# Performance work log

Hardware: AMD Instinct MI355X
Metric: run time of the kernel (lower is better)

The kernel has to match this reference:

```python
import jax, jax.numpy as jnp
import numpy as np

N_NODES = 50000
N_EDGES = 800000
D_IN = 128
D_HID = 128
D_OUT = 64


def sage_conv(x, edge_index, W_l, b_l, W_r):
    # PyG SAGEConv (mean aggr): out = lin_l(mean_{j in N(i)} x_j) + lin_r(x_i)
    src, dst = edge_index[0], edge_index[1]
    msgs = x[src]  # [E, d] gather of source-node features
    summed = jax.ops.segment_sum(msgs, dst, num_segments=x.shape[0])
    deg = jax.ops.segment_sum(jnp.ones((edge_index.shape[1],), x.dtype), dst,
                              num_segments=x.shape[0])
    agg = summed / jnp.maximum(deg, 1.0)[:, None]  # nodes w/o in-edges -> 0
    return agg @ W_l + b_l + x @ W_r


def setup_inputs() -> dict:
    key = jax.random.key(0)
    ks = jax.random.split(key, 12)
    x = jax.random.normal(ks[0], (N_NODES, D_IN), dtype=jnp.float32)
    edge_index = jax.random.randint(ks[1], (2, N_EDGES), 0, N_NODES, dtype=jnp.int32)

    def glorot(k, shape):
        fan_in, fan_out = shape
        lim = (6.0 / (fan_in + fan_out)) ** 0.5
        return jax.random.uniform(k, shape, jnp.float32, -lim, lim)

    dims = [(D_IN, D_HID), (D_HID, D_HID), (D_HID, D_OUT)]
    params = {}
    for i, (din, dout) in enumerate(dims):
        params[f"Wl{i}"] = glorot(ks[2 + 3 * i], (din, dout))
        params[f"bl{i}"] = jnp.zeros((dout,), jnp.float32)
        params[f"Wr{i}"] = glorot(ks[3 + 3 * i], (din, dout))
    return {"x": x, "edge_index": edge_index, **params}


def reference(x, edge_index, Wl0, bl0, Wr0, Wl1, bl1, Wr1, Wl2, bl2, Wr2):
    # eval mode: dropout is identity
    h = jax.nn.relu(sage_conv(x, edge_index, Wl0, bl0, Wr0))
    h = jax.nn.relu(sage_conv(h, edge_index, Wl1, bl1, Wr1))
    out = sage_conv(h, edge_index, Wl2, bl2, Wr2)
    return out
```

## Files before the change

### kernel.cpp

```cpp
#include <hip/hip_runtime.h>

#define NN 50000
#define NE 800000
#define DK 128
#define NN_PAD 50048

#define SW 7
#define SUBCAP 20
#define CAP2 64

#define NPB 128
#define NBKT 391
#define BKTCAP 4096

#define GEMM_GRID 391

typedef __attribute__((ext_vector_type(8))) short bf16x8;
typedef __attribute__((ext_vector_type(4))) float f32x4;
typedef __attribute__((ext_vector_type(2))) int   i32x2;
typedef __attribute__((ext_vector_type(4))) int   i32x4;
typedef __attribute__((ext_vector_type(4))) unsigned u32x4;
typedef __attribute__((ext_vector_type(8))) unsigned short u16x8;

__device__ inline unsigned short f2bf(float f) {
    unsigned u = __builtin_bit_cast(unsigned, f);
    u = (u + 0x7FFFu + ((u >> 16) & 1u)) >> 16;
    return (unsigned short)u;
}
__device__ inline float bfhi2f(unsigned u) {
    return __builtin_bit_cast(float, u & 0xFFFF0000u);
}
__device__ inline float bflo2f(unsigned u) {
    return __builtin_bit_cast(float, u << 16);
}
__device__ inline int clampn(int v) {
    return v >= NN ? NN - 1 : v;
}
__device__ inline void acc16(float* acc, u32x4 v) {
    acc[0] += bflo2f(v.x); acc[1] += bfhi2f(v.x);
    acc[2] += bflo2f(v.y); acc[3] += bfhi2f(v.y);
    acc[4] += bflo2f(v.z); acc[5] += bfhi2f(v.z);
    acc[6] += bflo2f(v.w); acc[7] += bfhi2f(v.w);
}
__device__ inline int xcd_swz(int b, int nwg) {
    int q = nwg >> 3, r = nwg & 7;
    int xc = b & 7, y = b >> 3;
    return (xc < r ? xc * (q + 1) : r * (q + 1) + (xc - r) * q) + y;
}


__global__ __launch_bounds__(256) void partition_edges(const int* __restrict__ src,
                                                       const int* __restrict__ dst,
                                                       int* __restrict__ gcount,
                                                       unsigned* __restrict__ bucketbuf) {
    __shared__ int hist[NBKT];
    __shared__ int cur[NBKT];
    __shared__ int base[NBKT];
    int tid = threadIdx.x;
    for (int i = tid; i < NBKT; i += 256) { hist[i] = 0; cur[i] = 0; }
    __syncthreads();

    unsigned rec[8];
    int bkt[8];
    int e0 = (blockIdx.x * 256 + tid) * 8;
    bool valid = e0 < NE;
    if (valid) {
        i32x4 sa = __builtin_nontemporal_load((const i32x4*)(src + e0));
        i32x4 sb = __builtin_nontemporal_load((const i32x4*)(src + e0 + 4));
        i32x4 da = __builtin_nontemporal_load((const i32x4*)(dst + e0));
        i32x4 db = __builtin_nontemporal_load((const i32x4*)(dst + e0 + 4));
        int ss[8] = {sa.x, sa.y, sa.z, sa.w, sb.x, sb.y, sb.z, sb.w};
        int dd[8] = {da.x, da.y, da.z, da.w, db.x, db.y, db.z, db.w};
        #pragma unroll
        for (int k = 0; k < 8; ++k) {
            bkt[k] = dd[k] >> 7;
            rec[k] = (unsigned)ss[k] | ((unsigned)(dd[k] & 127) << 16);
            atomicAdd(&hist[bkt[k]], 1);
        }
    }
    __syncthreads();
    for (int i = tid; i < NBKT; i += 256)
        base[i] = atomicAdd(&gcount[i], hist[i]);
    __syncthreads();
    if (valid) {
        #pragma unroll
        for (int k = 0; k < 8; ++k) {
            int pos = base[bkt[k]] + atomicAdd(&cur[bkt[k]], 1);
            if (pos < BKTCAP)
                bucketbuf[(size_t)bkt[k] * BKTCAP + pos] = rec[k];
        }
    }
}

__global__ __launch_bounds__(256) void build_lists(const int* __restrict__ gcount,
                                                   const unsigned* __restrict__ bucketbuf,
                                                   unsigned short* __restrict__ eidx2,
                                                   int* __restrict__ deg) {
    __shared__ unsigned short list[NPB * CAP2];
    __shared__ int cnt[NPB * 8];
    __shared__ int cur[NPB * 8];
    __shared__ int off_[NPB * 8];
    int b = blockIdx.x, tid = threadIdx.x;
    int n0 = b << 7;
    int cntE = gcount[b];
    if (cntE > BKTCAP) cntE = BKTCAP;

    for (int i = tid; i < NPB * 8; i += 256) { cnt[i] = 0; cur[i] = 0; }
    u32x4* l4 = (u32x4*)list;
    for (int i = tid; i < NPB * CAP2 / 8; i += 256)
        l4[i] = (u32x4){0u, 0u, 0u, 0u};
    __syncthreads();

    const unsigned* bb = bucketbuf + (size_t)b * BKTCAP;
    for (int i = tid; i < cntE; i += 256) {
        unsigned r = bb[i];
        int nl = r >> 16;
        int w  = (r & 0xFFFFu) >> 13;
        atomicAdd(&cnt[nl * 8 + w], 1);
    }
    __syncthreads();

    if (tid < NPB) {
        int run = 0, dt = 0;
        #pragma unroll
        for (int w = 0; w < SW; ++w) {
            int c = cnt[tid * 8 + w];
            dt += c;
            off_[tid * 8 + w] = run;
            run += (c < SUBCAP) ? c : SUBCAP;
        }
        if (n0 + tid < NN) deg[n0 + tid] = dt;
    }
    __syncthreads();

    for (int i = tid; i < cntE; i += 256) {
        unsigned r = bb[i];
        int s  = (int)(r & 0xFFFFu);
        int nl = r >> 16;
        int w  = s >> 13;
        int slot = atomicAdd(&cur[nl * 8 + w], 1);
        int pos  = off_[nl * 8 + w] + slot;
        if (slot < SUBCAP && pos < CAP2)
            list[nl * CAP2 + pos] = (unsigned short)s;
    }
    __syncthreads();

    int nvalid = NN - n0;
    if (nvalid > NPB) nvalid = NPB;
    u32x4* out4 = (u32x4*)(eidx2 + (size_t)n0 * CAP2);
    for (int i = tid; i < nvalid * (CAP2 / 8); i += 256)
        __builtin_nontemporal_store(l4[i], out4 + i);
}

__global__ __launch_bounds__(256) void prep(const float* __restrict__ x,
                                            unsigned short* __restrict__ xb,
                                            const float* __restrict__ Wl0,
                                            const float* __restrict__ Wr0,
                                            unsigned short* __restrict__ Wp0,
                                            const float* __restrict__ Wl1,
                                            const float* __restrict__ Wr1,
                                            unsigned short* __restrict__ Wp1,
                                            const float* __restrict__ Wl2,
                                            unsigned short* __restrict__ Wp2l,
                                            const float* __restrict__ Wr2,
                                            unsigned short* __restrict__ Wp2r,
                                            int* __restrict__ gcount) {
    int b = blockIdx.x;
    if (b < NN_PAD * DK / 8 / 256) {
        long long i = ((long long)b * 256 + threadIdx.x) * 8;
        if (i < (long long)NN * DK) {
            f32x4 a = __builtin_nontemporal_load((const f32x4*)(x + i));
            f32x4 c = __builtin_nontemporal_load((const f32x4*)(x + i + 4));
            union { unsigned short us[8]; u32x4 u4; } o;
            o.us[0] = f2bf(a.x); o.us[1] = f2bf(a.y); o.us[2] = f2bf(a.z); o.us[3] = f2bf(a.w);
            o.us[4] = f2bf(c.x); o.us[5] = f2bf(c.y); o.us[6] = f2bf(c.z); o.us[7] = f2bf(c.w);
            *(u32x4*)(xb + i) = o.u4;
        } else {
            *(u32x4*)(xb + i) = (u32x4){0u, 0u, 0u, 0u};
        }
        return;
    }
    b -= NN_PAD * DK / 8 / 256;
    if (b < 32) {
        const float* Wl = (b < 16) ? Wl0 : Wl1;
        const float* Wr = (b < 16) ? Wr0 : Wr1;
        unsigned short* Wp = (b < 16) ? Wp0 : Wp1;
        int tid = (b & 15) * 256 + threadIdx.x;
        int l  = tid & 63;
        int ks = (tid >> 6) & 7;
        int nt = tid >> 9;
        int n  = nt * 16 + (l & 15);
        int kb = ks * 32 + (l >> 4) * 8;
        union { unsigned short us[8]; u32x4 u4; } o;
        #pragma unroll
        for (int j = 0; j < 8; ++j) {
            int k = kb + j;
            float w = (k < 128) ? Wl[k * 128 + n] : Wr[(k - 128) * 128 + n];
            o.us[j] = f2bf(w);
        }
        *(u32x4*)(Wp + (size_t)tid * 8) = o.u4;
        return;
    }
    b -= 32;
    if (b < 8) {
        const float* W = (b < 4) ? Wl2 : Wr2;
        unsigned short* Wp = (b < 4) ? Wp2l : Wp2r;
        int tid = (b & 3) * 256 + threadIdx.x;
        int l  = tid & 63;
        int ks = (tid >> 6) & 3;
        int nt = tid >> 8;
        int n  = nt * 16 + (l & 15);
        int kb = ks * 32 + (l >> 4) * 8;
        union { unsigned short us[8]; u32x4 u4; } o;
        #pragma unroll
        for (int j = 0; j < 8; ++j) o.us[j] = f2bf(W[(kb + j) * 64 + n]);
        *(u32x4*)(Wp + (size_t)tid * 8) = o.u4;
        return;
    }
    for (int i = threadIdx.x; i < NBKT; i += 256) gcount[i] = 0;
}

template <bool P2OUT>
__global__ __launch_bounds__(256) void fused_layer(const unsigned short* __restrict__ h,
                                                   const unsigned short* __restrict__ eidx2,
                                                   const int* __restrict__ deg,
                                                   const unsigned short* __restrict__ Wpack,
                                                   const float* __restrict__ bias,
                                                   unsigned short* __restrict__ out,
                                                   const unsigned short* __restrict__ Wp2,
                                                   unsigned short* __restrict__ P2) {
    constexpr int RS = 136;
    __shared__ unsigned short Alds[128 * RS];
    int tid = threadIdx.x;
    int bid = xcd_swz(blockIdx.x, GEMM_GRID);
    int node0 = bid * 128;

    {
        int g = tid >> 4, lane = tid & 15;
        const u32x4* h4 = (const u32x4*)h;
        for (int pass = 0; pass < 8; ++pass) {
            int nl = pass * 16 + g;
            int node = node0 + nl;
            int d = (node < NN) ? deg[node] : 0;
            int cap = (d < CAP2) ? d : CAP2;
            const unsigned short* el = eidx2 + (size_t)node * CAP2;
            float acc[8] = {0.f, 0.f, 0.f, 0.f, 0.f, 0.f, 0.f, 0.f};
            int j = 0;
            for (; j + 7 < cap; j += 8) {
                u16x8 i8 = *(const u16x8*)(el + j);
                u32x4 v[8];
                #pragma unroll
                for (int q = 0; q < 8; ++q)
                    v[q] = h4[(size_t)clampn((int)i8[q]) * 16 + lane];
                #pragma unroll
                for (int q = 0; q < 8; ++q) acc16(acc, v[q]);
            }
            for (; j + 3 < cap; j += 4) {
                u32x4 v[4];
                #pragma unroll
                for (int q = 0; q < 4; ++q)
                    v[q] = h4[(size_t)clampn((int)el[j + q]) * 16 + lane];
                #pragma unroll
                for (int q = 0; q < 4; ++q) acc16(acc, v[q]);
            }
            for (; j < cap; ++j)
                acc16(acc, h4[(size_t)clampn((int)el[j]) * 16 + lane]);
            float rd = 1.0f / (float)(d > 0 ? d : 1);
            union { unsigned short us[8]; u32x4 u4; } o;
            #pragma unroll
            for (int k = 0; k < 8; ++k) o.us[k] = f2bf(acc[k] * rd);
            *(u32x4*)&Alds[nl * RS + lane * 8] = o.u4;
        }
    }
    __syncthreads();

    int wave = tid >> 6, lane = tid & 63;
    int m = lane & 15, quad = lane >> 4;
    int r0 = wave * 16;
    const unsigned short* a0p  = &Alds[(r0 + m) * RS + quad * 8];
    const unsigned short* hrow = h + (size_t)(node0 + r0 + m) * 128 + quad * 8;

    f32x4 acc0[8] = {};
    f32x4 acc1[8] = {};
    #pragma unroll
    for (int ks = 0; ks < 8; ++ks) {
        bf16x8 a0, a1;
        if (ks < 4) {
            a0 = *(const bf16x8*)(a0p + ks * 32);
            a1 = *(const bf16x8*)(a0p + 64 * RS + ks * 32);
        } else {
            a0 = *(const bf16x8*)(hrow + (ks - 4) * 32);
            a1 = *(const bf16x8*)(hrow + 64 * 128 + (ks - 4) * 32);
        }
        #pragma unroll
        for (int nt = 0; nt < 8; ++nt) {
            bf16x8 bfr = *(const bf16x8*)&Wpack[((size_t)(nt * 8 + ks) * 64 + lane) * 8];
            acc0[nt] = __builtin_amdgcn_mfma_f32_16x16x32_bf16(a0, bfr, acc0[nt], 0, 0, 0);
            acc1[nt] = __builtin_amdgcn_mfma_f32_16x16x32_bf16(a1, bfr, acc1[nt], 0, 0, 0);
        }
    }

    #pragma unroll
    for (int t = 0; t < 2; ++t) {
        #pragma unroll
        for (int nt = 0; nt < 8; ++nt) {
            int n = nt * 16 + m;
            float bv = bias[n];
            #pragma unroll
            for (int r = 0; r < 4; ++r) {
                int rl = t * 64 + r0 + quad * 4 + r;
                float v = fmaxf((t == 0 ? acc0[nt][r] : acc1[nt][r]) + bv, 0.f);
                unsigned short us = f2bf(v);
                out[(size_t)(node0 + rl) * 128 + n] = us;
                if constexpr (P2OUT) Alds[rl * RS + n] = us;
            }
        }
    }

    if constexpr (P2OUT) {
        f32x4 p0[4] = {};
        f32x4 p1[4] = {};
        #pragma unroll
        for (int ks = 0; ks < 4; ++ks) {
            bf16x8 a0 = *(const bf16x8*)&Alds[(r0 + m) * RS + ks * 32 + quad * 8];
            bf16x8 a1 = *(const bf16x8*)&Alds[(64 + r0 + m) * RS + ks * 32 + quad * 8];
            #pragma unroll
            for (int nt = 0; nt < 4; ++nt) {
                bf16x8 bfr = *(const bf16x8*)&Wp2[((size_t)(nt * 4 + ks) * 64 + lane) * 8];
                p0[nt] = __builtin_amdgcn_mfma_f32_16x16x32_bf16(a0, bfr, p0[nt], 0, 0, 0);
                p1[nt] = __builtin_amdgcn_mfma_f32_16x16x32_bf16(a1, bfr, p1[nt], 0, 0, 0);
            }
        }
        #pragma unroll
        for (int t = 0; t < 2; ++t) {
            #pragma unroll
            for (int nt = 0; nt < 4; ++nt) {
                int n = nt * 16 + m;
                #pragma unroll
                for (int r = 0; r < 4; ++r) {
                    int rl = t * 64 + r0 + quad * 4 + r;
                    P2[(size_t)(node0 + rl) * 64 + n] =
                        f2bf(t == 0 ? p0[nt][r] : p1[nt][r]);
                }
            }
        }
    }
}

__global__ __launch_bounds__(256) void fused_final(const unsigned short* __restrict__ h,
                                                   const unsigned short* __restrict__ P2,
                                                   const unsigned short* __restrict__ eidx2,
                                                   const int* __restrict__ deg,
                                                   const unsigned short* __restrict__ Wp2r,
                                                   const float* __restrict__ bias,
                                                   float* __restrict__ outp) {
    constexpr int RS2 = 72;
    __shared__ unsigned short Plds[128 * RS2];
    int tid = threadIdx.x;
    int bid = xcd_swz(blockIdx.x, GEMM_GRID);
    int node0 = bid * 128;

    {
        int g = tid >> 3, lane = tid & 7;
        const u32x4* p4 = (const u32x4*)P2;
        for (int pass = 0; pass < 4; ++pass) {
            int nl = pass * 32 + g;
            int node = node0 + nl;
            int d = (node < NN) ? deg[node] : 0;
            int cap = (d < CAP2) ? d : CAP2;
            const unsigned short* el = eidx2 + (size_t)node * CAP2;
            float acc[8] = {0.f, 0.f, 0.f, 0.f, 0.f, 0.f, 0.f, 0.f};
            int j = 0;
            for (; j + 7 < cap; j += 8) {
                u16x8 i8 = *(const u16x8*)(el + j);
                u32x4 v[8];
                #pragma unroll
                for (int q = 0; q < 8; ++q)
                    v[q] = p4[(size_t)clampn((int)i8[q]) * 8 + lane];
                #pragma unroll
                for (int q = 0; q < 8; ++q) acc16(acc, v[q]);
            }
            for (; j + 3 < cap; j += 4) {
                u32x4 v[4];
                #pragma unroll
                for (int q = 0; q < 4; ++q)
                    v[q] = p4[(size_t)clampn((int)el[j + q]) * 8 + lane];
                #pragma unroll
                for (int q = 0; q < 4; ++q) acc16(acc, v[q]);
            }
            for (; j < cap; ++j)
                acc16(acc, p4[(size_t)clampn((int)el[j]) * 8 + lane]);
            float rd = 1.0f / (float)(d > 0 ? d : 1);
            union { unsigned short us[8]; u32x4 u4; } o;
            #pragma unroll
            for (int k = 0; k < 8; ++k) o.us[k] = f2bf(acc[k] * rd);
            *(u32x4*)&Plds[nl * RS2 + lane * 8] = o.u4;
        }
    }
    __syncthreads();

    int wave = tid >> 6, lane = tid & 63;
    int m = lane & 15, quad = lane >> 4;
    int r0 = wave * 16;
    const unsigned short* hrow = h + (size_t)(node0 + r0 + m) * 128 + quad * 8;

    f32x4 acc0[4] = {};
    f32x4 acc1[4] = {};
    #pragma unroll
    for (int ks = 0; ks < 4; ++ks) {
        bf16x8 a0 = *(const bf16x8*)(hrow + ks * 32);
        bf16x8 a1 = *(const bf16x8*)(hrow + ks * 32 + 64 * 128);
        #pragma unroll
        for (int nt = 0; nt < 4; ++nt) {
            bf16x8 bfr = *(const bf16x8*)&Wp2r[((size_t)(nt * 4 + ks) * 64 + lane) * 8];
            acc0[nt] = __builtin_amdgcn_mfma_f32_16x16x32_bf16(a0, bfr, acc0[nt], 0, 0, 0);
            acc1[nt] = __builtin_amdgcn_mfma_f32_16x16x32_bf16(a1, bfr, acc1[nt], 0, 0, 0);
        }
    }

    #pragma unroll
    for (int t = 0; t < 2; ++t) {
        #pragma unroll
        for (int nt = 0; nt < 4; ++nt) {
            int n = nt * 16 + m;
            float bv = bias[n];
            #pragma unroll
            for (int r = 0; r < 4; ++r) {
                int rl = t * 64 + r0 + quad * 4 + r;
                int row = node0 + rl;
                if (row < NN) {
                    float av = bflo2f((unsigned)Plds[rl * RS2 + n]);
                    outp[(size_t)row * 64 + n] =
                        (t == 0 ? acc0[nt][r] : acc1[nt][r]) + bv + av;
                }
            }
        }
    }
}


static inline size_t align256(size_t x) { return (x + 255) & ~(size_t)255; }

extern "C" void kernel_launch(void* const* d_in, const int* in_sizes, int n_in,
                              void* d_out, int out_size, void* d_ws, size_t ws_size,
                              hipStream_t stream) {
    const float* x    = (const float*)d_in[0];
    const int*   ei   = (const int*)d_in[1];
    const int*   esrc = ei;
    const int*   edst = ei + NE;
    const float* Wl0 = (const float*)d_in[2];
    const float* bl0 = (const float*)d_in[3];
    const float* Wr0 = (const float*)d_in[4];
    const float* Wl1 = (const float*)d_in[5];
    const float* bl1 = (const float*)d_in[6];
    const float* Wr1 = (const float*)d_in[7];
    const float* Wl2 = (const float*)d_in[8];
    const float* bl2 = (const float*)d_in[9];
    const float* Wr2 = (const float*)d_in[10];

    char* ws = (char*)d_ws;
    size_t off = 0;
    int* gcount = (int*)(ws + off);             off = align256(off + (size_t)NBKT * 4);
    unsigned* bucketbuf = (unsigned*)(ws + off);
    off = align256(off + (size_t)NBKT * BKTCAP * 4);
    unsigned short* eidx2 = (unsigned short*)(ws + off);
    off = align256(off + (size_t)NN * CAP2 * 2);
    int* deg = (int*)(ws + off);                off = align256(off + (size_t)NN * 4);
    unsigned short* xb   = (unsigned short*)(ws + off); off = align256(off + (size_t)NN_PAD * DK * 2);
    unsigned short* bH   = (unsigned short*)(ws + off); off = align256(off + (size_t)NN_PAD * DK * 2);
    unsigned short* P2   = (unsigned short*)(ws + off); off = align256(off + (size_t)NN_PAD * 64 * 2);
    unsigned short* Wp0  = (unsigned short*)(ws + off); off = align256(off + (size_t)256 * 128 * 2);
    unsigned short* Wp1  = (unsigned short*)(ws + off); off = align256(off + (size_t)256 * 128 * 2);
    unsigned short* Wp2l = (unsigned short*)(ws + off); off = align256(off + (size_t)128 * 64 * 2);
    unsigned short* Wp2r = (unsigned short*)(ws + off); off = align256(off + (size_t)128 * 64 * 2);

    prep<<<NN_PAD * DK / 8 / 256 + 32 + 8 + 1, 256, 0, stream>>>(
        x, xb, Wl0, Wr0, Wp0, Wl1, Wr1, Wp1, Wl2, Wp2l, Wr2, Wp2r, gcount);
    partition_edges<<<(NE / 8 + 255) / 256, 256, 0, stream>>>(esrc, edst, gcount, bucketbuf);
    build_lists<<<NBKT, 256, 0, stream>>>(gcount, bucketbuf, eidx2, deg);

    fused_layer<false><<<GEMM_GRID, 256, 0, stream>>>(xb, eidx2, deg, Wp0, bl0, bH,
                                                      nullptr, nullptr);
    fused_layer<true><<<GEMM_GRID, 256, 0, stream>>>(bH, eidx2, deg, Wp1, bl1, xb,
                                                     Wp2l, P2);
    fused_final<<<GEMM_GRID, 256, 0, stream>>>(xb, P2, eidx2, deg, Wp2r, bl2,
                                               (float*)d_out);
}
```

Measured before the change: 272.1 us.

## Split fused gather+GEMM layers into separate aggregate and GEMM kernels

Each layer's fused gather-then-MFMA kernel is split in two: a dedicated aggregation kernel with more blocks (1568) that writes mean-aggregated bf16 features to a new global buffer, then a GEMM kernel that stages the packed weights in LDS and reads both aggregated and self features from global memory. The aim is more parallelism and better latency hiding for the irregular gather, which in the fused version ran on only 391 blocks, and less repeated weight traffic from global memory. In exchange it adds extra kernel launches and a round trip of the aggregated tensors through HBM, and it drops the XCD block swizzle.

```diff
diff --git a/kernel.cpp b/kernel.cpp
--- a/kernel.cpp
+++ b/kernel.cpp
@@ -14,6 +14,8 @@
 #define BKTCAP 4096
 
 #define GEMM_GRID 391
+
+#define AGG_BLOCKS 1568
 
 typedef __attribute__((ext_vector_type(8))) short bf16x8;
 typedef __attribute__((ext_vector_type(4))) float f32x4;
@@ -41,11 +43,6 @@
     acc[2] += bflo2f(v.y); acc[3] += bfhi2f(v.y);
     acc[4] += bflo2f(v.z); acc[5] += bfhi2f(v.z);
     acc[6] += bflo2f(v.w); acc[7] += bfhi2f(v.w);
-}
-__device__ inline int xcd_swz(int b, int nwg) {
-    int q = nwg >> 3, r = nwg & 7;
-    int xc = b & 7, y = b >> 3;
-    return (xc < r ? xc * (q + 1) : r * (q + 1) + (xc - r) * q) + y;
 }
 
 
@@ -220,83 +217,89 @@
     for (int i = threadIdx.x; i < NBKT; i += 256) gcount[i] = 0;
 }
 
+template <int S>
+__global__ __launch_bounds__(256) void aggregate(const unsigned short* __restrict__ h,
+                                                 const unsigned short* __restrict__ eidx2,
+                                                 const int* __restrict__ deg,
+                                                 unsigned short* __restrict__ agg) {
+    constexpr int NPB_ = 256 / S;
+    int g    = threadIdx.x / S;
+    int lane = threadIdx.x % S;
+    const u32x4* h4 = (const u32x4*)h;
+    for (int base = 0; base < NN; base += AGG_BLOCKS * NPB_) {
+        int node = base + blockIdx.x * NPB_ + g;
+        if (node >= NN) continue;
+        int d   = deg[node];
+        int cap = (d < CAP2) ? d : CAP2;
+        const unsigned short* el = eidx2 + (size_t)node * CAP2;
+        float acc[8] = {0.f, 0.f, 0.f, 0.f, 0.f, 0.f, 0.f, 0.f};
+        int j = 0;
+        for (; j + 7 < cap; j += 8) {
+            u16x8 i8 = *(const u16x8*)(el + j);
+            u32x4 v[8];
+            #pragma unroll
+            for (int q = 0; q < 8; ++q)
+                v[q] = h4[(size_t)clampn((int)i8[q]) * S + lane];
+            #pragma unroll
+            for (int q = 0; q < 8; ++q) acc16(acc, v[q]);
+        }
+        for (; j + 3 < cap; j += 4) {
+            u32x4 v[4];
+            #pragma unroll
+            for (int q = 0; q < 4; ++q)
+                v[q] = h4[(size_t)clampn((int)el[j + q]) * S + lane];
+            #pragma unroll
+            for (int q = 0; q < 4; ++q) acc16(acc, v[q]);
+        }
+        for (; j < cap; ++j)
+            acc16(acc, h4[(size_t)clampn((int)el[j]) * S + lane]);
+        float r = 1.0f / (float)(d > 0 ? d : 1);
+        union { unsigned short us[8]; u32x4 u4; } o;
+        #pragma unroll
+        for (int k = 0; k < 8; ++k) o.us[k] = f2bf(acc[k] * r);
+        __builtin_nontemporal_store(o.u4, (u32x4*)agg + (size_t)node * S + lane);
+    }
+}
+
+
 template <bool P2OUT>
-__global__ __launch_bounds__(256) void fused_layer(const unsigned short* __restrict__ h,
-                                                   const unsigned short* __restrict__ eidx2,
-                                                   const int* __restrict__ deg,
-                                                   const unsigned short* __restrict__ Wpack,
-                                                   const float* __restrict__ bias,
-                                                   unsigned short* __restrict__ out,
-                                                   const unsigned short* __restrict__ Wp2,
-                                                   unsigned short* __restrict__ P2) {
-    constexpr int RS = 136;
-    __shared__ unsigned short Alds[128 * RS];
+__global__ __launch_bounds__(256) void gemm_mfma(const unsigned short* __restrict__ agg,
+                                                 const unsigned short* __restrict__ h,
+                                                 const unsigned short* __restrict__ Wpack,
+                                                 const float* __restrict__ bias,
+                                                 unsigned short* __restrict__ out,
+                                                 const unsigned short* __restrict__ Wp2,
+                                                 unsigned short* __restrict__ P2) {
+    __shared__ unsigned short Wlds[128 * 256];
     int tid = threadIdx.x;
-    int bid = xcd_swz(blockIdx.x, GEMM_GRID);
-    int node0 = bid * 128;
-
     {
-        int g = tid >> 4, lane = tid & 15;
-        const u32x4* h4 = (const u32x4*)h;
-        for (int pass = 0; pass < 8; ++pass) {
-            int nl = pass * 16 + g;
-            int node = node0 + nl;
-            int d = (node < NN) ? deg[node] : 0;
-            int cap = (d < CAP2) ? d : CAP2;
-            const unsigned short* el = eidx2 + (size_t)node * CAP2;
-            float acc[8] = {0.f, 0.f, 0.f, 0.f, 0.f, 0.f, 0.f, 0.f};
-            int j = 0;
-            for (; j + 7 < cap; j += 8) {
-                u16x8 i8 = *(const u16x8*)(el + j);
-                u32x4 v[8];
-                #pragma unroll
-                for (int q = 0; q < 8; ++q)
-                    v[q] = h4[(size_t)clampn((int)i8[q]) * 16 + lane];
-                #pragma unroll
-                for (int q = 0; q < 8; ++q) acc16(acc, v[q]);
-            }
-            for (; j + 3 < cap; j += 4) {
-                u32x4 v[4];
-                #pragma unroll
-                for (int q = 0; q < 4; ++q)
-                    v[q] = h4[(size_t)clampn((int)el[j + q]) * 16 + lane];
-                #pragma unroll
-                for (int q = 0; q < 4; ++q) acc16(acc, v[q]);
-            }
-            for (; j < cap; ++j)
-                acc16(acc, h4[(size_t)clampn((int)el[j]) * 16 + lane]);
-            float rd = 1.0f / (float)(d > 0 ? d : 1);
-            union { unsigned short us[8]; u32x4 u4; } o;
-            #pragma unroll
-            for (int k = 0; k < 8; ++k) o.us[k] = f2bf(acc[k] * rd);
-            *(u32x4*)&Alds[nl * RS + lane * 8] = o.u4;
-        }
+        const u32x4* wg = (const u32x4*)Wpack;
+        u32x4* wl = (u32x4*)Wlds;
+        #pragma unroll
+        for (int i = tid; i < 128 * 32; i += 256) wl[i] = wg[i];
     }
     __syncthreads();
 
     int wave = tid >> 6, lane = tid & 63;
     int m = lane & 15, quad = lane >> 4;
     int r0 = wave * 16;
-    const unsigned short* a0p  = &Alds[(r0 + m) * RS + quad * 8];
-    const unsigned short* hrow = h + (size_t)(node0 + r0 + m) * 128 + quad * 8;
+    int row0 = blockIdx.x * 128 + r0;
+
+    const unsigned short* arow = agg + (size_t)(row0 + m) * 128 + quad * 8;
+    const unsigned short* hrow = h   + (size_t)(row0 + m) * 128 + quad * 8;
 
     f32x4 acc0[8] = {};
     f32x4 acc1[8] = {};
     #pragma unroll
     for (int ks = 0; ks < 8; ++ks) {
-        bf16x8 a0, a1;
-        if (ks < 4) {
-            a0 = *(const bf16x8*)(a0p + ks * 32);
-            a1 = *(const bf16x8*)(a0p + 64 * RS + ks * 32);
-        } else {
-            a0 = *(const bf16x8*)(hrow + (ks - 4) * 32);
-            a1 = *(const bf16x8*)(hrow + 64 * 128 + (ks - 4) * 32);
-        }
+        const unsigned short* s = (ks < 4) ? (arow + ks * 32) : (hrow + (ks - 4) * 32);
+        bf16x8 a0 = *(const bf16x8*)s;
+        bf16x8 a1 = *(const bf16x8*)(s + 64 * 128);
         #pragma unroll
         for (int nt = 0; nt < 8; ++nt) {
-            bf16x8 bfr = *(const bf16x8*)&Wpack[((size_t)(nt * 8 + ks) * 64 + lane) * 8];
-            acc0[nt] = __builtin_amdgcn_mfma_f32_16x16x32_bf16(a0, bfr, acc0[nt], 0, 0, 0);
-            acc1[nt] = __builtin_amdgcn_mfma_f32_16x16x32_bf16(a1, bfr, acc1[nt], 0, 0, 0);
+            bf16x8 b = *(const bf16x8*)&Wlds[((nt * 8 + ks) * 64 + lane) * 8];
+            acc0[nt] = __builtin_amdgcn_mfma_f32_16x16x32_bf16(a0, b, acc0[nt], 0, 0, 0);
+            acc1[nt] = __builtin_amdgcn_mfma_f32_16x16x32_bf16(a1, b, acc1[nt], 0, 0, 0);
         }
     }
 
@@ -308,22 +311,38 @@
             float bv = bias[n];
             #pragma unroll
             for (int r = 0; r < 4; ++r) {
-                int rl = t * 64 + r0 + quad * 4 + r;
-                float v = fmaxf((t == 0 ? acc0[nt][r] : acc1[nt][r]) + bv, 0.f);
-                unsigned short us = f2bf(v);
-                out[(size_t)(node0 + rl) * 128 + n] = us;
-                if constexpr (P2OUT) Alds[rl * RS + n] = us;
+                int row = row0 + t * 64 + quad * 4 + r;
+                if (row < NN) {
+                    float v = fmaxf((t == 0 ? acc0[nt][r] : acc1[nt][r]) + bv, 0.f);
+                    out[(size_t)row * 128 + n] = f2bf(v);
+                }
             }
         }
     }
 
     if constexpr (P2OUT) {
+        constexpr int RS = 136;
+        __syncthreads();
+        #pragma unroll
+        for (int t = 0; t < 2; ++t) {
+            #pragma unroll
+            for (int nt = 0; nt < 8; ++nt) {
+                int n = nt * 16 + m;
+                float bv = bias[n];
+                #pragma unroll
+                for (int r = 0; r < 4; ++r) {
+                    int rl = t * 64 + r0 + quad * 4 + r;
+                    float v = fmaxf((t == 0 ? acc0[nt][r] : acc1[nt][r]) + bv, 0.f);
+                    Wlds[rl * RS + n] = f2bf(v);
+                }
+            }
+        }
         f32x4 p0[4] = {};
         f32x4 p1[4] = {};
         #pragma unroll
         for (int ks = 0; ks < 4; ++ks) {
-            bf16x8 a0 = *(const bf16x8*)&Alds[(r0 + m) * RS + ks * 32 + quad * 8];
-            bf16x8 a1 = *(const bf16x8*)&Alds[(64 + r0 + m) * RS + ks * 32 + quad * 8];
+            bf16x8 a0 = *(const bf16x8*)&Wlds[(r0 + m) * RS + ks * 32 + quad * 8];
+            bf16x8 a1 = *(const bf16x8*)&Wlds[(64 + r0 + m) * RS + ks * 32 + quad * 8];
             #pragma unroll
             for (int nt = 0; nt < 4; ++nt) {
                 bf16x8 bfr = *(const bf16x8*)&Wp2[((size_t)(nt * 4 + ks) * 64 + lane) * 8];
@@ -339,7 +358,7 @@
                 #pragma unroll
                 for (int r = 0; r < 4; ++r) {
                     int rl = t * 64 + r0 + quad * 4 + r;
-                    P2[(size_t)(node0 + rl) * 64 + n] =
+                    P2[(size_t)(blockIdx.x * 128 + rl) * 64 + n] =
                         f2bf(t == 0 ? p0[nt][r] : p1[nt][r]);
                 }
             }
@@ -347,62 +366,26 @@
     }
 }
 
-__global__ __launch_bounds__(256) void fused_final(const unsigned short* __restrict__ h,
-                                                   const unsigned short* __restrict__ P2,
-                                                   const unsigned short* __restrict__ eidx2,
-                                                   const int* __restrict__ deg,
-                                                   const unsigned short* __restrict__ Wp2r,
-                                                   const float* __restrict__ bias,
-                                                   float* __restrict__ outp) {
-    constexpr int RS2 = 72;
-    __shared__ unsigned short Plds[128 * RS2];
+__global__ __launch_bounds__(256) void gemm_final(const unsigned short* __restrict__ h,
+                                                  const unsigned short* __restrict__ Wpack,
+                                                  const float* __restrict__ bias,
+                                                  const unsigned short* __restrict__ aggP,
+                                                  float* __restrict__ outp) {
+    __shared__ unsigned short Wlds[64 * 128];
     int tid = threadIdx.x;
-    int bid = xcd_swz(blockIdx.x, GEMM_GRID);
-    int node0 = bid * 128;
-
     {
-        int g = tid >> 3, lane = tid & 7;
-        const u32x4* p4 = (const u32x4*)P2;
-        for (int pass = 0; pass < 4; ++pass) {
-            int nl = pass * 32 + g;
-            int node = node0 + nl;
-            int d = (node < NN) ? deg[node] : 0;
-            int cap = (d < CAP2) ? d : CAP2;
-            const unsigned short* el = eidx2 + (size_t)node * CAP2;
-            float acc[8] = {0.f, 0.f, 0.f, 0.f, 0.f, 0.f, 0.f, 0.f};
-            int j = 0;
-            for (; j + 7 < cap; j += 8) {
-                u16x8 i8 = *(const u16x8*)(el + j);
-                u32x4 v[8];
-                #pragma unroll
-                for (int q = 0; q < 8; ++q)
-                    v[q] = p4[(size_t)clampn((int)i8[q]) * 8 + lane];
-                #pragma unroll
-                for (int q = 0; q < 8; ++q) acc16(acc, v[q]);
-            }
-            for (; j + 3 < cap; j += 4) {
-                u32x4 v[4];
-                #pragma unroll
-                for (int q = 0; q < 4; ++q)
-                    v[q] = p4[(size_t)clampn((int)el[j + q]) * 8 + lane];
-                #pragma unroll
-                for (int q = 0; q < 4; ++q) acc16(acc, v[q]);
-            }
-            for (; j < cap; ++j)
-                acc16(acc, p4[(size_t)clampn((int)el[j]) * 8 + lane]);
-            float rd = 1.0f / (float)(d > 0 ? d : 1);
-            union { unsigned short us[8]; u32x4 u4; } o;
-            #pragma unroll
-            for (int k = 0; k < 8; ++k) o.us[k] = f2bf(acc[k] * rd);
-            *(u32x4*)&Plds[nl * RS2 + lane * 8] = o.u4;
-        }
+        const u32x4* wg = (const u32x4*)Wpack;
+        u32x4* wl = (u32x4*)Wlds;
+        #pragma unroll
+        for (int i = tid; i < 1024; i += 256) wl[i] = wg[i];
     }
     __syncthreads();
 
     int wave = tid >> 6, lane = tid & 63;
     int m = lane & 15, quad = lane >> 4;
-    int r0 = wave * 16;
-    const unsigned short* hrow = h + (size_t)(node0 + r0 + m) * 128 + quad * 8;
+    int row0 = blockIdx.x * 128 + wave * 16;
+
+    const unsigned short* hrow = h + (size_t)(row0 + m) * 128 + quad * 8;
 
     f32x4 acc0[4] = {};
     f32x4 acc1[4] = {};
@@ -412,9 +395,9 @@
         bf16x8 a1 = *(const bf16x8*)(hrow + ks * 32 + 64 * 128);
         #pragma unroll
         for (int nt = 0; nt < 4; ++nt) {
-            bf16x8 bfr = *(const bf16x8*)&Wp2r[((size_t)(nt * 4 + ks) * 64 + lane) * 8];
-            acc0[nt] = __builtin_amdgcn_mfma_f32_16x16x32_bf16(a0, bfr, acc0[nt], 0, 0, 0);
-            acc1[nt] = __builtin_amdgcn_mfma_f32_16x16x32_bf16(a1, bfr, acc1[nt], 0, 0, 0);
+            bf16x8 b = *(const bf16x8*)&Wlds[((nt * 4 + ks) * 64 + lane) * 8];
+            acc0[nt] = __builtin_amdgcn_mfma_f32_16x16x32_bf16(a0, b, acc0[nt], 0, 0, 0);
+            acc1[nt] = __builtin_amdgcn_mfma_f32_16x16x32_bf16(a1, b, acc1[nt], 0, 0, 0);
         }
     }
 
@@ -426,10 +409,9 @@
             float bv = bias[n];
             #pragma unroll
             for (int r = 0; r < 4; ++r) {
-                int rl = t * 64 + r0 + quad * 4 + r;
-                int row = node0 + rl;
+                int row = row0 + t * 64 + quad * 4 + r;
                 if (row < NN) {
-                    float av = bflo2f((unsigned)Plds[rl * RS2 + n]);
+                    float av = bflo2f((unsigned)aggP[(size_t)row * 64 + n]);
                     outp[(size_t)row * 64 + n] =
                         (t == 0 ? acc0[nt][r] : acc1[nt][r]) + bv + av;
                 }
@@ -467,8 +449,10 @@
     off = align256(off + (size_t)NN * CAP2 * 2);
     int* deg = (int*)(ws + off);                off = align256(off + (size_t)NN * 4);
     unsigned short* xb   = (unsigned short*)(ws + off); off = align256(off + (size_t)NN_PAD * DK * 2);
+    unsigned short* bAgg = (unsigned short*)(ws + off); off = align256(off + (size_t)NN_PAD * DK * 2);
     unsigned short* bH   = (unsigned short*)(ws + off); off = align256(off + (size_t)NN_PAD * DK * 2);
     unsigned short* P2   = (unsigned short*)(ws + off); off = align256(off + (size_t)NN_PAD * 64 * 2);
+    unsigned short* aggP = (unsigned short*)(ws + off); off = align256(off + (size_t)NN_PAD * 64 * 2);
     unsigned short* Wp0  = (unsigned short*)(ws + off); off = align256(off + (size_t)256 * 128 * 2);
     unsigned short* Wp1  = (unsigned short*)(ws + off); off = align256(off + (size_t)256 * 128 * 2);
     unsigned short* Wp2l = (unsigned short*)(ws + off); off = align256(off + (size_t)128 * 64 * 2);
@@ -479,10 +463,14 @@
     partition_edges<<<(NE / 8 + 255) / 256, 256, 0, stream>>>(esrc, edst, gcount, bucketbuf);
     build_lists<<<NBKT, 256, 0, stream>>>(gcount, bucketbuf, eidx2, deg);
 
-    fused_layer<false><<<GEMM_GRID, 256, 0, stream>>>(xb, eidx2, deg, Wp0, bl0, bH,
-                                                      nullptr, nullptr);
-    fused_layer<true><<<GEMM_GRID, 256, 0, stream>>>(bH, eidx2, deg, Wp1, bl1, xb,
-                                                     Wp2l, P2);
-    fused_final<<<GEMM_GRID, 256, 0, stream>>>(xb, P2, eidx2, deg, Wp2r, bl2,
-                                               (float*)d_out);
-}
+    aggregate<16><<<AGG_BLOCKS, 256, 0, stream>>>(xb, eidx2, deg, bAgg);
+    gemm_mfma<false><<<GEMM_GRID, 256, 0, stream>>>(bAgg, xb, Wp0, bl0, bH,
+                                                    nullptr, nullptr);
+
+    aggregate<16><<<AGG_BLOCKS, 256, 0, stream>>>(bH, eidx2, deg, bAgg);
+    gemm_mfma<true><<<GEMM_GRID, 256, 0, stream>>>(bAgg, bH, Wp1, bl1, xb,
+                                                   Wp2l, P2);
+
+    aggregate<8><<<AGG_BLOCKS, 256, 0, stream>>>(P2, eidx2, deg, aggP);
+    gemm_final<<<GEMM_GRID, 256, 0, stream>>>(xb, Wp2r, bl2, aggP, (float*)d_out);
+}
```

After: 240.1 us. 1.13x faster.
